# Kernel optimization log

Hardware: AMD Instinct MI355X
Metric: run time of the kernel (lower is better)

Reference implementation:

```python
import jax, jax.numpy as jnp
import numpy as np

EMBED = 1024
HEADS = 16
HEAD_DIM = EMBED // HEADS


def setup_inputs() -> dict:
    key = jax.random.key(0)
    ks = jax.random.split(key, 9)
    B, S = 2, 2048
    values = jax.random.normal(ks[0], (B, S, EMBED), dtype=jnp.float32)
    keys_in = jax.random.normal(ks[1], (B, S, EMBED), dtype=jnp.float32)
    query = jax.random.normal(ks[2], (B, S, EMBED), dtype=jnp.float32)
    mask = jax.random.randint(ks[3], (B, 1, 1, S), 0, 2, dtype=jnp.int32)
    # torch Linear weights: [out_features, in_features], y = x @ W.T
    sc = 1.0 / np.sqrt(HEAD_DIM)
    Wv = jax.random.uniform(ks[4], (HEAD_DIM, HEAD_DIM), jnp.float32, -sc, sc)
    Wk = jax.random.uniform(ks[5], (HEAD_DIM, HEAD_DIM), jnp.float32, -sc, sc)
    Wq = jax.random.uniform(ks[6], (HEAD_DIM, HEAD_DIM), jnp.float32, -sc, sc)
    so = 1.0 / np.sqrt(EMBED)
    Wo = jax.random.uniform(ks[7], (EMBED, EMBED), jnp.float32, -so, so)
    bo = jax.random.uniform(ks[8], (EMBED,), jnp.float32, -so, so)
    return {"values": values, "keys": keys_in, "query": query, "mask": mask,
            "Wv": Wv, "Wk": Wk, "Wq": Wq, "Wo": Wo, "bo": bo}


def reference(values, keys, query, mask, Wv, Wk, Wq, Wo, bo):
    B = query.shape[0]
    # split heads: [B, S, H, D]
    v = values.reshape(B, -1, HEADS, HEAD_DIM)
    k = keys.reshape(B, -1, HEADS, HEAD_DIM)
    q = query.reshape(B, -1, HEADS, HEAD_DIM)
    # per-head shared linear projections (nn.Linear on last dim, no bias)
    v = jnp.einsum('bshd,ed->bshe', v, Wv)
    k = jnp.einsum('bshd,ed->bshe', k, Wk)
    q = jnp.einsum('bshd,ed->bshe', q, Wq)
    # energy: [B, H, Q, K]
    energy = jnp.einsum('bqhd,bkhd->bhqk', q, k)
    energy = jnp.where(mask == 0, jnp.float32(-1e20), energy)
    attn = jax.nn.softmax(energy / jnp.sqrt(jnp.float32(EMBED)), axis=3)
    out = jnp.einsum('bhqk,bkhd->bqhd', attn, v).reshape(B, -1, EMBED)
    return out @ Wo.T + bo
```

## Files before the change

kernel.cpp:

```cpp
#include <hip/hip_runtime.h>
#include <hip/hip_bf16.h>


typedef __attribute__((ext_vector_type(8))) short bf16x8;
typedef __attribute__((ext_vector_type(4))) float f32x4;
typedef __attribute__((ext_vector_type(16))) float f32x16;
typedef __attribute__((ext_vector_type(2))) int i32x2;

__device__ int g_srcidx[2 * 2048];
__device__ int g_NK[2];

__device__ __forceinline__ short f2bf(float x) {
  union { float f; unsigned u; } v; v.f = x;
  unsigned r = v.u + 0x7FFFu + ((v.u >> 16) & 1u);
  return (short)(r >> 16);
}

__device__ __forceinline__ int pack2(float lo, float hi) {
  __hip_bfloat162 h = __float22bfloat162_rn(make_float2(lo, hi));
  int r; __builtin_memcpy(&r, &h, 4); return r;
}

__device__ __forceinline__ bf16x8 cvt8(float4 a, float4 b) {
  union { int i[4]; bf16x8 h; } u;
  u.i[0] = pack2(a.x, a.y);
  u.i[1] = pack2(a.z, a.w);
  u.i[2] = pack2(b.x, b.y);
  u.i[3] = pack2(b.z, b.w);
  return u.h;
}

__device__ __forceinline__ void plsw(int& a, int& b) {
  i32x2 r = __builtin_amdgcn_permlane32_swap(a, b, false, false);
  a = r[0]; b = r[1];
}
__device__ __forceinline__ float pl_comb_add(float v) {
  int a = __float_as_int(v), b = a;
  i32x2 r = __builtin_amdgcn_permlane32_swap(a, b, false, false);
  return __int_as_float(r[0]) + __int_as_float(r[1]);
}

__device__ __forceinline__ void gll16(const short* g, short* l) {
  __builtin_amdgcn_global_load_lds(
      (const __attribute__((address_space(1))) void*)g,
      (__attribute__((address_space(3))) void*)l, 16, 0, 0);
}

__global__ __launch_bounds__(256) void prep_kernel(
    const int* __restrict__ mask, const float* __restrict__ Wo,
    short* __restrict__ WoB) {
  __shared__ int cnt[256];
  const int t = threadIdx.x;
  if (blockIdx.x < 2) {
    const int b = blockIdx.x;
    const int* m = mask + b * 2048;
    int* sidx = g_srcidx + b * 2048;
    const int base = t * 8;
    int vals[8], lc = 0;
#pragma unroll
    for (int i = 0; i < 8; i++) { vals[i] = (m[base + i] != 0); lc += vals[i]; }
    cnt[t] = lc;
    __syncthreads();
    for (int off = 1; off < 256; off <<= 1) {
      int v = (t >= off) ? cnt[t - off] : 0;
      __syncthreads();
      cnt[t] += v;
      __syncthreads();
    }
    int pos = cnt[t] - lc;
    const int total = cnt[255];
#pragma unroll
    for (int i = 0; i < 8; i++)
      if (vals[i]) sidx[pos++] = base + i;
    for (int j = total + t; j < 2048; j += 256) sidx[j] = 0;
    if (t == 0) g_NK[b] = total;
  } else {
    int i = ((blockIdx.x - 2) * 256 + t) * 8;
    float4 a = *(const float4*)(Wo + i), b2 = *(const float4*)(Wo + i + 4);
    *(bf16x8*)(WoB + i) = cvt8(a, b2);
  }
}

__global__ __launch_bounds__(256) void proj_kernel(
    const float* __restrict__ keys, const float* __restrict__ query,
    const float* __restrict__ values,
    const float* __restrict__ Wk, const float* __restrict__ Wq,
    const float* __restrict__ Wv,
    short* __restrict__ Kp, short* __restrict__ Qp, short* __restrict__ Vt) {
  const int bid0 = blockIdx.x;
  const int t = threadIdx.x;
  const int w = t >> 6, l = t & 63, l15 = l & 15, l4 = l >> 4;
  __shared__ short Al[64 * 64];
  __shared__ short Bl[64 * 64];
  __shared__ short Tl[64 * 66];

  if (bid0 < 2048) {
    int bid = bid0;
    const float* X = keys; const float* W = Wk; short* O = Kp;
    bool isq = false;
    if (bid >= 1024) { X = query; W = Wq; O = Qp; bid -= 1024; isq = true; }
    const int r0 = bid << 6;
    const int bb = r0 >> 15;
    if (!isq) {
      const int j0 = (r0 >> 4) & 2047;
      const int jlim = (g_NK[bb] + 63) & ~63;
      if (j0 >= jlim) return;
    }
#pragma unroll
    for (int i = 0; i < 2; i++) {
      int c = t + (i << 8);
      int row = c >> 3, col8 = c & 7;
      int pc = col8 ^ (row & 7);
      int ri = r0 + row;
      int j = (ri >> 4) & 2047, hh = ri & 15;
      int s = isq ? j : g_srcidx[(bb << 11) + j];
      const float* xs = X + ((size_t)((bb * 2048 + s) * 16 + hh)) * 64 + col8 * 8;
      float4 a0 = *(const float4*)xs, a1 = *(const float4*)(xs + 4);
      *(bf16x8*)&Al[row * 64 + pc * 8] = cvt8(a0, a1);
      const float* wsrc = W + row * 64 + col8 * 8;
      float4 b0 = *(const float4*)wsrc, b1 = *(const float4*)(wsrc + 4);
      *(bf16x8*)&Bl[row * 64 + pc * 8] = cvt8(b0, b1);
    }
    __syncthreads();
    f32x4 acc[4];
#pragma unroll
    for (int i = 0; i < 4; i++) acc[i] = (f32x4){0.f, 0.f, 0.f, 0.f};
#pragma unroll
    for (int kc = 0; kc < 2; kc++) {
      int ar = w * 16 + l15;
      bf16x8 af = *(const bf16x8*)((const char*)Al +
          ((ar * 128 + kc * 64 + l4 * 16) ^ ((ar & 7) << 4)));
#pragma unroll
      for (int ng = 0; ng < 4; ng++) {
        int br = ng * 16 + l15;
        bf16x8 bfr = *(const bf16x8*)((const char*)Bl +
            ((br * 128 + kc * 64 + l4 * 16) ^ ((br & 7) << 4)));
        acc[ng] = __builtin_amdgcn_mfma_f32_16x16x32_bf16(af, bfr, acc[ng], 0, 0, 0);
      }
    }
    const float osc = isq ? (1.4426950408889634f / 32.0f) : 1.0f;
#pragma unroll
    for (int ng = 0; ng < 4; ng++) {
#pragma unroll
      for (int j = 0; j < 4; j++) {
        int ri = r0 + w * 16 + l4 * 4 + j;
        int e = ng * 16 + l15;
        int b2 = ri >> 15, jj = (ri >> 4) & 2047, hh = ri & 15;
        O[(((size_t)(b2 * 16 + hh)) * 2048 + jj) * 64 + e] = f2bf(acc[ng][j] * osc);
      }
    }
  } else {
    const int bid = bid0 - 2048;
    const int st = bid & 31, bh = bid >> 5;
    const int b = bh >> 4, h = bh & 15;
    const int s0 = st << 6;
    const int jlim = (g_NK[b] + 63) & ~63;
    if (s0 >= jlim) return;
#pragma unroll
    for (int i = 0; i < 2; i++) {
      int c = t + (i << 8);
      int row = c >> 3, col8 = c & 7;
      int pc = col8 ^ (row & 7);
      int s = g_srcidx[(b << 11) + s0 + row];
      const float* xs = values + ((size_t)(b * 2048 + s)) * 1024 + h * 64 + col8 * 8;
      float4 a0 = *(const float4*)xs, a1 = *(const float4*)(xs + 4);
      *(bf16x8*)&Al[row * 64 + pc * 8] = cvt8(a0, a1);
      const float* wsrc = Wv + row * 64 + col8 * 8;
      float4 b0 = *(const float4*)wsrc, b1 = *(const float4*)(wsrc + 4);
      *(bf16x8*)&Bl[row * 64 + pc * 8] = cvt8(b0, b1);
    }
    __syncthreads();
    f32x4 acc[4];
#pragma unroll
    for (int i = 0; i < 4; i++) acc[i] = (f32x4){0.f, 0.f, 0.f, 0.f};
#pragma unroll
    for (int kc = 0; kc < 2; kc++) {
      int ar = w * 16 + l15;
      bf16x8 af = *(const bf16x8*)((const char*)Al +
          ((ar * 128 + kc * 64 + l4 * 16) ^ ((ar & 7) << 4)));
#pragma unroll
      for (int ng = 0; ng < 4; ng++) {
        int br = ng * 16 + l15;
        bf16x8 bfr = *(const bf16x8*)((const char*)Bl +
            ((br * 128 + kc * 64 + l4 * 16) ^ ((br & 7) << 4)));
        acc[ng] = __builtin_amdgcn_mfma_f32_16x16x32_bf16(af, bfr, acc[ng], 0, 0, 0);
      }
    }
#pragma unroll
    for (int ng = 0; ng < 4; ng++) {
#pragma unroll
      for (int j = 0; j < 4; j++) {
        Tl[(w * 16 + l4 * 4 + j) * 66 + ng * 16 + l15] = f2bf(acc[ng][j]);
      }
    }
    __syncthreads();
    int e = t >> 2, sc = (t & 3) << 4;
    bf16x8 o0, o1;
#pragma unroll
    for (int i = 0; i < 8; i++) {
      o0[i] = Tl[(sc + i) * 66 + e];
      o1[i] = Tl[(sc + 8 + i) * 66 + e];
    }
    short* dst = Vt + ((size_t)bh * 64 + e) * 2048 + s0 + sc;
    *(bf16x8*)dst = o0;
    *(bf16x8*)(dst + 8) = o1;
  }
}

__global__ __launch_bounds__(256, 2) void attn_kernel(
    const short* __restrict__ Qp, const short* __restrict__ Kp,
    const short* __restrict__ Vt, short* __restrict__ AO) {
  const int bid = (int)(blockIdx.x % 8) * 64 + (int)(blockIdx.x / 8);
  const int qb = bid & 15, bh = bid >> 4;
  const int b = bh >> 4, h = bh & 15;
  const int t = threadIdx.x;
  const int w = t >> 6, l = t & 63, l31 = l & 31, hi = l >> 5;
  const int q0w = qb * 128 + w * 32;

  __shared__ short Kl[2][64 * 64];
  __shared__ short Vl[2][64 * 64];
  __shared__ float Cl[4 * 32];

  const short* Kbase = Kp + (size_t)bh * 2048 * 64;
  const short* Vbase = Vt + (size_t)bh * 64 * 2048;

  const int nk = g_NK[b];
  const int ntiles = (nk + 63) >> 6;

  const short* qptr = Qp + ((size_t)bh * 2048 + q0w + l31) * 64 + hi * 8;
  bf16x8 qf[4];
#pragma unroll
  for (int dc = 0; dc < 4; dc++) qf[dc] = *(const bf16x8*)(qptr + dc * 16);

  int laddr[2][4];
#pragma unroll
  for (int x = 0; x < 2; x++) {
    int rr = x * 32 + l31;
#pragma unroll
    for (int c2 = 0; c2 < 4; c2++)
      laddr[x][c2] = rr * 128 + (((c2 * 32) + hi * 16) ^ ((rr & 7) << 4));
  }

  const int srow = t >> 3, scol = t & 7;
  const int sc0 = (scol ^ (srow & 7)) * 8;
  const short* ksrc0 = Kbase + srow * 64 + sc0;
  const short* ksrc1 = Kbase + (srow + 32) * 64 + sc0;
  const short* vsrc0 = Vbase + (size_t)srow * 2048 + sc0;
  const short* vsrc1 = Vbase + (size_t)(srow + 32) * 2048 + sc0;
  short* klds = &Kl[0][0];
  short* vlds = &Vl[0][0];
  const int d0 = t * 8, d1 = t * 8 + 2048;

  gll16(ksrc0, klds + d0);
  gll16(ksrc1, klds + d1);
  gll16(vsrc0, vlds + d0);
  gll16(vsrc1, vlds + d1);
  __syncthreads();

  float l_run = 0.f;
  f32x16 o0, o1;
#pragma unroll
  for (int r = 0; r < 16; r++) { o0[r] = 0.f; o1[r] = 0.f; }

  for (int kt = 0; kt < ntiles; kt++) {
    const int bs = kt & 1;
    const int bsb = bs << 13;
    if (kt + 1 < ntiles) {
      const int nb = (bs ^ 1) << 12;
      gll16(ksrc0 + (kt + 1) * 4096, klds + nb + d0);
      gll16(ksrc1 + (kt + 1) * 4096, klds + nb + d1);
      gll16(vsrc0 + (kt + 1) * 64, vlds + nb + d0);
      gll16(vsrc1 + (kt + 1) * 64, vlds + nb + d1);
    }

    f32x16 st0, st1;
#pragma unroll
    for (int r = 0; r < 16; r++) { st0[r] = 0.f; st1[r] = 0.f; }
    __builtin_amdgcn_s_setprio(1);
#pragma unroll
    for (int dc = 0; dc < 4; dc++) {
      bf16x8 ka = *(const bf16x8*)((const char*)Kl + bsb + laddr[0][dc]);
      st0 = __builtin_amdgcn_mfma_f32_32x32x16_bf16(ka, qf[dc], st0, 0, 0, 0);
    }
#pragma unroll
    for (int dc = 0; dc < 4; dc++) {
      bf16x8 kb = *(const bf16x8*)((const char*)Kl + bsb + laddr[1][dc]);
      st1 = __builtin_amdgcn_mfma_f32_32x32x16_bf16(kb, qf[dc], st1, 0, 0, 0);
    }
    __builtin_amdgcn_s_setprio(0);

    if (((kt << 6) + 64) <= nk) {
#pragma unroll
      for (int r = 0; r < 16; r++) {
        st0[r] = __builtin_amdgcn_exp2f(st0[r]);
        st1[r] = __builtin_amdgcn_exp2f(st1[r]);
      }
    } else {
      const int kb2 = kt << 6;
#pragma unroll
      for (int r = 0; r < 16; r++) {
        int cr = (r & 3) + 8 * (r >> 2) + 4 * hi;
        float e0 = __builtin_amdgcn_exp2f(st0[r]);
        float e1 = __builtin_amdgcn_exp2f(st1[r]);
        st0[r] = (kb2 + cr < nk) ? e0 : 0.f;
        st1[r] = (kb2 + 32 + cr < nk) ? e1 : 0.f;
      }
    }

    float sx[8];
#pragma unroll
    for (int i = 0; i < 8; i++)
      sx[i] = (st0[2 * i] + st0[2 * i + 1]) + (st1[2 * i] + st1[2 * i + 1]);
#pragma unroll
    for (int s2 = 4; s2 > 0; s2 >>= 1)
#pragma unroll
      for (int i = 0; i < 4; i++)
        if (i < s2) sx[i] += sx[i + s2];
    l_run += pl_comb_add(sx[0]);

    bf16x8 pa[4];
#pragma unroll
    for (int kc = 0; kc < 4; kc++) {
      int bse = (kc & 1) * 8;
      float p0, p1, p2, p3, p4, p5, p6, p7;
      if (kc < 2) {
        p0 = st0[bse + 0]; p1 = st0[bse + 1]; p2 = st0[bse + 2]; p3 = st0[bse + 3];
        p4 = st0[bse + 4]; p5 = st0[bse + 5]; p6 = st0[bse + 6]; p7 = st0[bse + 7];
      } else {
        p0 = st1[bse + 0]; p1 = st1[bse + 1]; p2 = st1[bse + 2]; p3 = st1[bse + 3];
        p4 = st1[bse + 4]; p5 = st1[bse + 5]; p6 = st1[bse + 6]; p7 = st1[bse + 7];
      }
      int A0 = pack2(p0, p1), A1 = pack2(p2, p3);
      int B0 = pack2(p4, p5), B1 = pack2(p6, p7);
      plsw(A0, B0);
      plsw(A1, B1);
      union { int4 i; bf16x8 h; } u;
      u.i = make_int4(A0, A1, B0, B1);
      pa[kc] = u.h;
    }

    __builtin_amdgcn_s_setprio(1);
#pragma unroll
    for (int kc = 0; kc < 4; kc++) {
      bf16x8 vf = *(const bf16x8*)((const char*)Vl + bsb + laddr[0][kc]);
      o0 = __builtin_amdgcn_mfma_f32_32x32x16_bf16(pa[kc], vf, o0, 0, 0, 0);
    }
#pragma unroll
    for (int kc = 0; kc < 4; kc++) {
      bf16x8 vf = *(const bf16x8*)((const char*)Vl + bsb + laddr[1][kc]);
      o1 = __builtin_amdgcn_mfma_f32_32x32x16_bf16(pa[kc], vf, o1, 0, 0, 0);
    }
    __builtin_amdgcn_s_setprio(0);
    __syncthreads();
  }

  float invr = 1.0f / l_run;
  Cl[w * 32 + l31] = invr;
  short* aob = AO + ((size_t)(b * 2048 + q0w)) * 1024 + h * 64 + l31;
#pragma unroll
  for (int r = 0; r < 16; r++) {
    int qr = (r & 3) + 8 * (r >> 2) + 4 * hi;
    float ic = Cl[w * 32 + qr];
    aob[(size_t)qr * 1024] = f2bf(o0[r] * ic);
    aob[(size_t)qr * 1024 + 32] = f2bf(o1[r] * ic);
  }
}

__global__ __launch_bounds__(256) void outproj_kernel(
    const short* __restrict__ AO, const short* __restrict__ WoB,
    const float* __restrict__ bo, float* __restrict__ Cout) {
  const int bid = (int)(blockIdx.x % 8) * 128 + (int)(blockIdx.x / 8);
  const int mt = bid >> 4, nt = bid & 15;
  const int m0 = mt << 6, n0 = nt << 6;
  const int t = threadIdx.x;
  const int w = t >> 6, l = t & 63, l15 = l & 15, l4 = l >> 4;
  __shared__ short Al[2][64 * 64];
  __shared__ short Bl[2][64 * 64];

  const int srow = t >> 3, scol = t & 7;
  const int sc0 = (scol ^ (srow & 7)) * 8;
  const short* asrc0 = AO + (size_t)(m0 + srow) * 1024 + sc0;
  const short* asrc1 = AO + (size_t)(m0 + srow + 32) * 1024 + sc0;
  const short* bsrc0 = WoB + (size_t)(n0 + srow) * 1024 + sc0;
  const short* bsrc1 = WoB + (size_t)(n0 + srow + 32) * 1024 + sc0;
  short* al = &Al[0][0];
  short* bl = &Bl[0][0];
  const int d0 = t * 8, d1 = t * 8 + 2048;

  gll16(asrc0, al + d0); gll16(asrc1, al + d1);
  gll16(bsrc0, bl + d0); gll16(bsrc1, bl + d1);
  __syncthreads();

  f32x4 acc[4];
#pragma unroll
  for (int i = 0; i < 4; i++) acc[i] = (f32x4){0.f, 0.f, 0.f, 0.f};

  for (int ks = 0; ks < 16; ks++) {
    const int bs = ks & 1, bsb = bs << 13;
    if (ks < 15) {
      const int nb = (bs ^ 1) << 12;
      const int ko = (ks + 1) * 64;
      gll16(asrc0 + ko, al + nb + d0); gll16(asrc1 + ko, al + nb + d1);
      gll16(bsrc0 + ko, bl + nb + d0); gll16(bsrc1 + ko, bl + nb + d1);
    }
#pragma unroll
    for (int kc = 0; kc < 2; kc++) {
      int ar = w * 16 + l15;
      bf16x8 af = *(const bf16x8*)((const char*)Al + bsb +
          ((ar * 128 + kc * 64 + l4 * 16) ^ ((ar & 7) << 4)));
#pragma unroll
      for (int ng = 0; ng < 4; ng++) {
        int br = ng * 16 + l15;
        bf16x8 bfr = *(const bf16x8*)((const char*)Bl + bsb +
            ((br * 128 + kc * 64 + l4 * 16) ^ ((br & 7) << 4)));
        acc[ng] = __builtin_amdgcn_mfma_f32_16x16x32_bf16(af, bfr, acc[ng], 0, 0, 0);
      }
    }
    __syncthreads();
  }
#pragma unroll
  for (int ng = 0; ng < 4; ng++) {
    int n = n0 + ng * 16 + l15;
    float bias = bo[n];
#pragma unroll
    for (int j = 0; j < 4; j++) {
      int m = m0 + w * 16 + l4 * 4 + j;
      Cout[(size_t)m * 1024 + n] = acc[ng][j] + bias;
    }
  }
}

extern "C" void kernel_launch(void* const* d_in, const int* in_sizes, int n_in,
                              void* d_out, int out_size, void* d_ws, size_t ws_size,
                              hipStream_t stream) {
  const float* values = (const float*)d_in[0];
  const float* keys   = (const float*)d_in[1];
  const float* query  = (const float*)d_in[2];
  const int*   mask   = (const int*)d_in[3];
  const float* Wv = (const float*)d_in[4];
  const float* Wk = (const float*)d_in[5];
  const float* Wq = (const float*)d_in[6];
  const float* Wo = (const float*)d_in[7];
  const float* bo = (const float*)d_in[8];
  float* out = (float*)d_out;
  char* ws = (char*)d_ws;
  short* Qp  = (short*)(ws + (size_t)0);
  short* Kp  = (short*)(ws + ((size_t)8 << 20));
  short* Vtp = (short*)(ws + ((size_t)16 << 20));
  short* AO  = (short*)(ws + ((size_t)24 << 20));
  short* WoB = (short*)(ws + ((size_t)32 << 20));

  prep_kernel<<<514, 256, 0, stream>>>(mask, Wo, WoB);
  proj_kernel<<<3072, 256, 0, stream>>>(keys, query, values, Wk, Wq, Wv, Kp, Qp, Vtp);
  attn_kernel<<<512, 256, 0, stream>>>(Qp, Kp, Vtp, AO);
  outproj_kernel<<<1024, 256, 0, stream>>>(AO, WoB, bo, out);
}
```

Measured before the change: 67.71 us.

## Deepen K/V LDS pipeline to four buffers with two tiles in flight

Replaces the double-buffered K/V LDS staging with a four-slot ring that prefetches two tiles ahead. Explicit vmcnt waits and a single barrier per iteration replace the trailing __syncthreads, so global loads overlap more compute. This doubles LDS use per block (64KB for K/V), which may reduce occupancy below two blocks per CU. It also relies on the vmcnt counts matching the number of outstanding async loads.

New measurement: 68.14 us. Within noise of the previous version (+0.6%).

```diff
diff --git a/kernel.cpp b/kernel.cpp
--- a/kernel.cpp
+++ b/kernel.cpp
@@ -217,8 +217,8 @@
   const int w = t >> 6, l = t & 63, l31 = l & 31, hi = l >> 5;
   const int q0w = qb * 128 + w * 32;
 
-  __shared__ short Kl[2][64 * 64];
-  __shared__ short Vl[2][64 * 64];
+  __shared__ short Kl[4][64 * 64];
+  __shared__ short Vl[4][64 * 64];
   __shared__ float Cl[4 * 32];
 
   const short* Kbase = Kp + (size_t)bh * 2048 * 64;
@@ -251,27 +251,35 @@
   short* vlds = &Vl[0][0];
   const int d0 = t * 8, d1 = t * 8 + 2048;
 
-  gll16(ksrc0, klds + d0);
-  gll16(ksrc1, klds + d1);
-  gll16(vsrc0, vlds + d0);
-  gll16(vsrc1, vlds + d1);
-  __syncthreads();
-
   float l_run = 0.f;
   f32x16 o0, o1;
 #pragma unroll
   for (int r = 0; r < 16; r++) { o0[r] = 0.f; o1[r] = 0.f; }
 
+  auto stage = [&](int kt) {
+    const int off = (kt & 3) << 12;
+    gll16(ksrc0 + kt * 4096, klds + off + d0);
+    gll16(ksrc1 + kt * 4096, klds + off + d1);
+    gll16(vsrc0 + kt * 64, vlds + off + d0);
+    gll16(vsrc1 + kt * 64, vlds + off + d1);
+  };
+
+  stage(0);
+  if (ntiles > 1) stage(1);
+
   for (int kt = 0; kt < ntiles; kt++) {
-    const int bs = kt & 1;
-    const int bsb = bs << 13;
-    if (kt + 1 < ntiles) {
-      const int nb = (bs ^ 1) << 12;
-      gll16(ksrc0 + (kt + 1) * 4096, klds + nb + d0);
-      gll16(ksrc1 + (kt + 1) * 4096, klds + nb + d1);
-      gll16(vsrc0 + (kt + 1) * 64, vlds + nb + d0);
-      gll16(vsrc1 + (kt + 1) * 64, vlds + nb + d1);
-    }
+    if (kt + 2 < ntiles) {
+      stage(kt + 2);
+      asm volatile("s_waitcnt vmcnt(8)" ::: "memory");
+    } else if (kt + 1 < ntiles) {
+      asm volatile("s_waitcnt vmcnt(4)" ::: "memory");
+    } else {
+      asm volatile("s_waitcnt vmcnt(0)" ::: "memory");
+    }
+    __builtin_amdgcn_s_barrier();
+    __builtin_amdgcn_sched_barrier(0);
+
+    const int bsb = (kt & 3) << 13;
 
     f32x16 st0, st1;
 #pragma unroll
@@ -351,9 +359,9 @@
       o1 = __builtin_amdgcn_mfma_f32_32x32x16_bf16(pa[kc], vf, o1, 0, 0, 0);
     }
     __builtin_amdgcn_s_setprio(0);
-    __syncthreads();
-  }
-
+  }
+
+  __syncthreads();
   float invr = 1.0f / l_run;
   Cl[w * 32 + l31] = invr;
   short* aob = AO + ((size_t)(b * 2048 + q0w)) * 1024 + h * 64 + l31;
```

## Enlarge out-projection tiles to 128x128 and move Wo conversion into projection kernel

Applied to the files above, without the earlier changes.

The output projection GEMM now uses 128x128 tiles with 512-thread blocks. Each wave computes a 64x32 sub-tile with 4x2 MFMA accumulators, which raises operand reuse from LDS and cuts global traffic, but only 256 blocks are launched. The Wo fp32-to-bf16 conversion moves from the prep kernel into extra blocks of the projection kernel, leaving prep as a tiny 2-block mask scan. The aim is less serialization in the short prep kernel and better GEMM efficiency, at the cost of fewer blocks, which may underfill the CUs, and higher register use.

Measured after the change: 65.39 us. 1.04x faster.

```diff
diff --git a/kernel.cpp b/kernel.cpp
--- a/kernel.cpp
+++ b/kernel.cpp
@@ -46,49 +46,48 @@
       (__attribute__((address_space(3))) void*)l, 16, 0, 0);
 }
 
-__global__ __launch_bounds__(256) void prep_kernel(
-    const int* __restrict__ mask, const float* __restrict__ Wo,
-    short* __restrict__ WoB) {
+__global__ __launch_bounds__(256) void prep_kernel(const int* __restrict__ mask) {
   __shared__ int cnt[256];
   const int t = threadIdx.x;
-  if (blockIdx.x < 2) {
-    const int b = blockIdx.x;
-    const int* m = mask + b * 2048;
-    int* sidx = g_srcidx + b * 2048;
-    const int base = t * 8;
-    int vals[8], lc = 0;
-#pragma unroll
-    for (int i = 0; i < 8; i++) { vals[i] = (m[base + i] != 0); lc += vals[i]; }
-    cnt[t] = lc;
-    __syncthreads();
-    for (int off = 1; off < 256; off <<= 1) {
-      int v = (t >= off) ? cnt[t - off] : 0;
-      __syncthreads();
-      cnt[t] += v;
-      __syncthreads();
-    }
-    int pos = cnt[t] - lc;
-    const int total = cnt[255];
-#pragma unroll
-    for (int i = 0; i < 8; i++)
-      if (vals[i]) sidx[pos++] = base + i;
-    for (int j = total + t; j < 2048; j += 256) sidx[j] = 0;
-    if (t == 0) g_NK[b] = total;
-  } else {
-    int i = ((blockIdx.x - 2) * 256 + t) * 8;
-    float4 a = *(const float4*)(Wo + i), b2 = *(const float4*)(Wo + i + 4);
-    *(bf16x8*)(WoB + i) = cvt8(a, b2);
-  }
+  const int b = blockIdx.x;
+  const int* m = mask + b * 2048;
+  int* sidx = g_srcidx + b * 2048;
+  const int base = t * 8;
+  int vals[8], lc = 0;
+#pragma unroll
+  for (int i = 0; i < 8; i++) { vals[i] = (m[base + i] != 0); lc += vals[i]; }
+  cnt[t] = lc;
+  __syncthreads();
+  for (int off = 1; off < 256; off <<= 1) {
+    int v = (t >= off) ? cnt[t - off] : 0;
+    __syncthreads();
+    cnt[t] += v;
+    __syncthreads();
+  }
+  int pos = cnt[t] - lc;
+  const int total = cnt[255];
+#pragma unroll
+  for (int i = 0; i < 8; i++)
+    if (vals[i]) sidx[pos++] = base + i;
+  for (int j = total + t; j < 2048; j += 256) sidx[j] = 0;
+  if (t == 0) g_NK[b] = total;
 }
 
 __global__ __launch_bounds__(256) void proj_kernel(
     const float* __restrict__ keys, const float* __restrict__ query,
     const float* __restrict__ values,
     const float* __restrict__ Wk, const float* __restrict__ Wq,
-    const float* __restrict__ Wv,
-    short* __restrict__ Kp, short* __restrict__ Qp, short* __restrict__ Vt) {
+    const float* __restrict__ Wv, const float* __restrict__ Wo,
+    short* __restrict__ Kp, short* __restrict__ Qp, short* __restrict__ Vt,
+    short* __restrict__ WoB) {
   const int bid0 = blockIdx.x;
   const int t = threadIdx.x;
+  if (bid0 >= 3072) {
+    int i = ((bid0 - 3072) * 256 + t) * 8;
+    float4 a = *(const float4*)(Wo + i), b2 = *(const float4*)(Wo + i + 4);
+    *(bf16x8*)(WoB + i) = cvt8(a, b2);
+    return;
+  }
   const int w = t >> 6, l = t & 63, l15 = l & 15, l4 = l >> 4;
   __shared__ short Al[64 * 64];
   __shared__ short Bl[64 * 64];
@@ -366,66 +365,89 @@
   }
 }
 
-__global__ __launch_bounds__(256) void outproj_kernel(
+__global__ __launch_bounds__(512) void outproj_kernel(
     const short* __restrict__ AO, const short* __restrict__ WoB,
     const float* __restrict__ bo, float* __restrict__ Cout) {
-  const int bid = (int)(blockIdx.x % 8) * 128 + (int)(blockIdx.x / 8);
-  const int mt = bid >> 4, nt = bid & 15;
-  const int m0 = mt << 6, n0 = nt << 6;
+  const int bid = (int)(blockIdx.x % 8) * 32 + (int)(blockIdx.x / 8);
+  const int mt = bid >> 3, nt = bid & 7;
+  const int m0 = mt << 7, n0 = nt << 7;
   const int t = threadIdx.x;
-  const int w = t >> 6, l = t & 63, l15 = l & 15, l4 = l >> 4;
-  __shared__ short Al[2][64 * 64];
-  __shared__ short Bl[2][64 * 64];
-
-  const int srow = t >> 3, scol = t & 7;
-  const int sc0 = (scol ^ (srow & 7)) * 8;
-  const short* asrc0 = AO + (size_t)(m0 + srow) * 1024 + sc0;
-  const short* asrc1 = AO + (size_t)(m0 + srow + 32) * 1024 + sc0;
-  const short* bsrc0 = WoB + (size_t)(n0 + srow) * 1024 + sc0;
-  const short* bsrc1 = WoB + (size_t)(n0 + srow + 32) * 1024 + sc0;
+  const int w = t >> 6, wr = w >> 2, wc = w & 3;
+  const int l = t & 63, l15 = l & 15, l4 = l >> 4;
+  __shared__ short Al[2][128 * 64];
+  __shared__ short Bl[2][128 * 64];
+
+  const short* asrc[2];
+  const short* bsrc[2];
+  int ldst[2];
+#pragma unroll
+  for (int i = 0; i < 2; i++) {
+    int c = t + (i << 9);
+    int row = c >> 3, col8 = c & 7;
+    int sc = (col8 ^ (row & 7)) * 8;
+    asrc[i] = AO + (size_t)(m0 + row) * 1024 + sc;
+    bsrc[i] = WoB + (size_t)(n0 + row) * 1024 + sc;
+    ldst[i] = c * 8;
+  }
   short* al = &Al[0][0];
   short* bl = &Bl[0][0];
-  const int d0 = t * 8, d1 = t * 8 + 2048;
-
-  gll16(asrc0, al + d0); gll16(asrc1, al + d1);
-  gll16(bsrc0, bl + d0); gll16(bsrc1, bl + d1);
+
+  auto stage = [&](int ks, int bs) {
+    const int nb = bs << 13;
+    const int ko = ks * 64;
+#pragma unroll
+    for (int i = 0; i < 2; i++) {
+      gll16(asrc[i] + ko, al + nb + ldst[i]);
+      gll16(bsrc[i] + ko, bl + nb + ldst[i]);
+    }
+  };
+
+  stage(0, 0);
   __syncthreads();
 
-  f32x4 acc[4];
-#pragma unroll
-  for (int i = 0; i < 4; i++) acc[i] = (f32x4){0.f, 0.f, 0.f, 0.f};
+  f32x4 acc[4][2];
+#pragma unroll
+  for (int mi = 0; mi < 4; mi++)
+#pragma unroll
+    for (int ni = 0; ni < 2; ni++) acc[mi][ni] = (f32x4){0.f, 0.f, 0.f, 0.f};
 
   for (int ks = 0; ks < 16; ks++) {
-    const int bs = ks & 1, bsb = bs << 13;
-    if (ks < 15) {
-      const int nb = (bs ^ 1) << 12;
-      const int ko = (ks + 1) * 64;
-      gll16(asrc0 + ko, al + nb + d0); gll16(asrc1 + ko, al + nb + d1);
-      gll16(bsrc0 + ko, bl + nb + d0); gll16(bsrc1 + ko, bl + nb + d1);
-    }
+    const int bs = ks & 1, bsb = bs << 14;
+    if (ks < 15) stage(ks + 1, bs ^ 1);
 #pragma unroll
     for (int kc = 0; kc < 2; kc++) {
-      int ar = w * 16 + l15;
-      bf16x8 af = *(const bf16x8*)((const char*)Al + bsb +
-          ((ar * 128 + kc * 64 + l4 * 16) ^ ((ar & 7) << 4)));
-#pragma unroll
-      for (int ng = 0; ng < 4; ng++) {
-        int br = ng * 16 + l15;
+      bf16x8 af[4];
+#pragma unroll
+      for (int mi = 0; mi < 4; mi++) {
+        int ar = wr * 64 + mi * 16 + l15;
+        af[mi] = *(const bf16x8*)((const char*)Al + bsb +
+            ((ar * 128 + kc * 64 + l4 * 16) ^ ((ar & 7) << 4)));
+      }
+#pragma unroll
+      for (int ni = 0; ni < 2; ni++) {
+        int br = wc * 32 + ni * 16 + l15;
         bf16x8 bfr = *(const bf16x8*)((const char*)Bl + bsb +
             ((br * 128 + kc * 64 + l4 * 16) ^ ((br & 7) << 4)));
-        acc[ng] = __builtin_amdgcn_mfma_f32_16x16x32_bf16(af, bfr, acc[ng], 0, 0, 0);
-      }
-    }
-    __syncthreads();
-  }
-#pragma unroll
-  for (int ng = 0; ng < 4; ng++) {
-    int n = n0 + ng * 16 + l15;
+#pragma unroll
+        for (int mi = 0; mi < 4; mi++)
+          acc[mi][ni] = __builtin_amdgcn_mfma_f32_16x16x32_bf16(
+              af[mi], bfr, acc[mi][ni], 0, 0, 0);
+      }
+    }
+    __syncthreads();
+  }
+
+#pragma unroll
+  for (int ni = 0; ni < 2; ni++) {
+    int n = n0 + wc * 32 + ni * 16 + l15;
     float bias = bo[n];
 #pragma unroll
-    for (int j = 0; j < 4; j++) {
-      int m = m0 + w * 16 + l4 * 4 + j;
-      Cout[(size_t)m * 1024 + n] = acc[ng][j] + bias;
+    for (int mi = 0; mi < 4; mi++) {
+#pragma unroll
+      for (int j = 0; j < 4; j++) {
+        int m = m0 + wr * 64 + mi * 16 + l4 * 4 + j;
+        Cout[(size_t)m * 1024 + n] = acc[mi][ni][j] + bias;
+      }
     }
   }
 }
@@ -450,8 +472,9 @@
   short* AO  = (short*)(ws + ((size_t)24 << 20));
   short* WoB = (short*)(ws + ((size_t)32 << 20));
 
-  prep_kernel<<<514, 256, 0, stream>>>(mask, Wo, WoB);
-  proj_kernel<<<3072, 256, 0, stream>>>(keys, query, values, Wk, Wq, Wv, Kp, Qp, Vtp);
+  prep_kernel<<<2, 256, 0, stream>>>(mask);
+  proj_kernel<<<3584, 256, 0, stream>>>(keys, query, values, Wk, Wq, Wv, Wo,
+                                        Kp, Qp, Vtp, WoB);
   attn_kernel<<<512, 256, 0, stream>>>(Qp, Kp, Vtp, AO);
-  outproj_kernel<<<1024, 256, 0, stream>>>(AO, WoB, bo, out);
-}
+  outproj_kernel<<<256, 512, 0, stream>>>(AO, WoB, bo, out);
+}
```
